# Kernel optimization log

Measured on AMD Instinct MI355X. Metric: run time of the kernel, lower is better.

Reference implementation:

```python
import jax, jax.numpy as jnp
import numpy as np

B, C, L = 16, 256, 4096
P, Q = 100, 20


def setup_inputs() -> dict:
    key = jax.random.key(0)
    k1, k2, k3, k4 = jax.random.split(key, 4)
    X = jax.random.normal(k1, (B, C, L), dtype=jnp.float32)
    projections = jax.random.normal(k2, (P, C), dtype=jnp.float32)
    # min < max per projection. Projected values ~ N(0, sqrt(C)), so scale ~ sqrt(C).
    scale = jnp.sqrt(jnp.float32(C))
    min_vals = -scale * (1.0 + jax.random.uniform(k3, (P,), dtype=jnp.float32))
    max_vals = scale * (1.0 + jax.random.uniform(k4, (P,), dtype=jnp.float32))
    return {"X": X, "projections": projections, "min_vals": min_vals, "max_vals": max_vals}


def reference(X, projections, min_vals, max_vals):
    # conv1d with kernel size 1 == per-position projection: [B,C,L] x [P,C] -> [B,P,L]
    a = jnp.einsum('bcl,pc->bpl', X, projections)
    # all quantile thresholds at once: thr[p,q] = min + (max-min)*(q+1)/(Q+1)
    fracs = (jnp.arange(1, Q + 1, dtype=jnp.float32)) / jnp.float32(Q + 1)  # [Q]
    thr = min_vals[:, None] + (max_vals - min_vals)[:, None] * fracs[None, :]  # [P,Q]
    # set[b,p,l,q] = a[b,p,l] < thr[p,q]
    set_ = (a[:, :, :, None] < thr[None, :, None, :]).astype(jnp.float32)  # [B,P,L,Q]
    cdf = jnp.mean(set_, axis=2)  # [B,P,Q]
    # transpose(2,1) -> [B,L,P,Q]; reshape -> [B,L,P*Q]; transpose(2,1) -> [B,P*Q,L]
    set_out = jnp.transpose(set_, (0, 2, 1, 3)).reshape(B, L, P * Q)
    set_out = jnp.transpose(set_out, (0, 2, 1))  # [B, P*Q, L]
    cdf_out = cdf.reshape(B, P * Q)
    return (cdf_out, set_out)
```

## Files before the change

kernel.cpp:

```cpp
#include <hip/hip_runtime.h>

#define Bsz 16
#define Cc  256
#define Ll  4096
#define Pp  100
#define Qq  20
#define PQ  (Pp * Qq)

#define LTILE 1024
#define NLT   (Ll / LTILE)
#define GP    10
#define NPG   (Pp / GP)
#define NXCD  8

typedef float f32x4 __attribute__((ext_vector_type(4)));

__global__ __launch_bounds__(256) void csf_main(
    const float* __restrict__ X,
    const float* __restrict__ proj,
    const float* __restrict__ mn,
    const float* __restrict__ mx,
    float* __restrict__ cdf,
    float* __restrict__ set_out) {
    const int id = blockIdx.x;
    const int x  = id & (NXCD - 1);
    const int k  = id >> 3;
    const int pg = k % NPG;
    const int gq = k / NPG;
    const int g  = gq * NXCD + x;
    const int lt = g & (NLT - 1);
    const int b  = g >> 2;

    const int tid = threadIdx.x;
    const int l0  = lt * LTILE + tid * 4;
    const int p0  = __builtin_amdgcn_readfirstlane(pg * GP);

    const float* Xb = X + (size_t)b * Cc * Ll + l0;

    float acc[GP][4];
#pragma unroll
    for (int i = 0; i < GP; i++)
#pragma unroll
        for (int kk = 0; kk < 4; kk++) acc[i][kk] = 0.0f;

#pragma unroll 4
    for (int c = 0; c < Cc; c++) {
        const f32x4 xv = *(const f32x4*)(Xb + (size_t)c * Ll);
#pragma unroll
        for (int i = 0; i < GP; i++) {
            const float w = proj[(size_t)(p0 + i) * Cc + c];
            acc[i][0] = __builtin_fmaf(xv.x, w, acc[i][0]);
            acc[i][1] = __builtin_fmaf(xv.y, w, acc[i][1]);
            acc[i][2] = __builtin_fmaf(xv.z, w, acc[i][2]);
            acc[i][3] = __builtin_fmaf(xv.w, w, acc[i][3]);
        }
    }

    float fr[Qq];
#pragma unroll
    for (int q = 0; q < Qq; q++) fr[q] = __fdiv_rn((float)(q + 1), 21.0f);

    float* ob = set_out + (size_t)b * PQ * Ll + l0;
    const bool lane0 = ((tid & 63) == 0);

#pragma unroll 1
    for (int i = 0; i < GP; i++) {
        const int p = p0 + i;
        const float mnp = mn[p];
        const float mxp = mx[p];
        const float d = __fsub_rn(mxp, mnp);
#pragma unroll
        for (int q = 0; q < Qq; q++) {
            const float thr = __fadd_rn(mnp, __fmul_rn(d, fr[q]));
            const bool b0 = acc[i][0] < thr;
            const bool b1 = acc[i][1] < thr;
            const bool b2 = acc[i][2] < thr;
            const bool b3 = acc[i][3] < thr;
            f32x4 o;
            o.x = b0 ? 1.0f : 0.0f;
            o.y = b1 ? 1.0f : 0.0f;
            o.z = b2 ? 1.0f : 0.0f;
            o.w = b3 ? 1.0f : 0.0f;
            __builtin_nontemporal_store(o, (f32x4*)(ob + (size_t)(p * Qq + q) * Ll));
            const int cnt = __popcll(__ballot(b0)) + __popcll(__ballot(b1))
                          + __popcll(__ballot(b2)) + __popcll(__ballot(b3));
            if (lane0) {
                atomicAdd(&cdf[(size_t)b * PQ + p * Qq + q],
                          (float)cnt * (1.0f / (float)Ll));
            }
        }
    }
}

extern "C" void kernel_launch(void* const* d_in, const int* in_sizes, int n_in,
                              void* d_out, int out_size, void* d_ws, size_t ws_size,
                              hipStream_t stream) {
    const float* X    = (const float*)d_in[0];
    const float* proj = (const float*)d_in[1];
    const float* mn   = (const float*)d_in[2];
    const float* mx   = (const float*)d_in[3];

    float* cdf     = (float*)d_out;
    float* set_out = cdf + (size_t)Bsz * PQ;

    (void)hipMemsetAsync(cdf, 0, (size_t)Bsz * PQ * sizeof(float), stream);

    csf_main<<<dim3(NLT * NPG * Bsz), 256, 0, stream>>>(X, proj, mn, mx, cdf,
                                                        set_out);
}
```

Baseline: 602.1 us.

## Split projection and thresholding into two kernels, stash projections in output buffer

Splits the fused kernel in two. The first kernel computes the projection and writes each value into the q=0 row of set_out, which serves as scratch space. The second kernel has one block per (b,p); it reads the full L row, writes all Q threshold rows, and reduces counts in shared memory into cdf with plain stores. This removes the memset and the per-wave atomics and gives full-row CDF reduction, but adds a write and re-read of the projections and a second launch. Reading row q=0 before overwriting it is safe only because each thread reads its own elements first.

```diff
diff --git a/kernel.cpp b/kernel.cpp
--- a/kernel.cpp
+++ b/kernel.cpp
@@ -15,96 +15,130 @@
 
 typedef float f32x4 __attribute__((ext_vector_type(4)));
 
-__global__ __launch_bounds__(256) void csf_main(
+
+__global__ __launch_bounds__(256) void csf_proj(
     const float* __restrict__ X,
     const float* __restrict__ proj,
+    float* __restrict__ set_out) {
+  const int id = blockIdx.x;
+  const int x  = id & (NXCD - 1);
+  const int k  = id >> 3;
+  const int pg = k % NPG;
+  const int gq = k / NPG;
+  const int g  = gq * NXCD + x;
+  const int lt = g & (NLT - 1);
+  const int b  = g >> 2;
+
+  const int tid = threadIdx.x;
+  const int l0  = lt * LTILE + tid * 4;
+  const int p0  = __builtin_amdgcn_readfirstlane(pg * GP);
+
+  const float* Xb = X + (size_t)b * Cc * Ll + l0;
+
+  float acc[GP][4];
+#pragma unroll
+  for (int i = 0; i < GP; i++)
+#pragma unroll
+    for (int kk = 0; kk < 4; kk++) acc[i][kk] = 0.0f;
+
+#pragma unroll 4
+  for (int c = 0; c < Cc; c++) {
+    const f32x4 xv = *(const f32x4*)(Xb + (size_t)c * Ll);
+#pragma unroll
+    for (int i = 0; i < GP; i++) {
+      const float w = proj[(size_t)(p0 + i) * Cc + c];
+      acc[i][0] = __builtin_fmaf(xv.x, w, acc[i][0]);
+      acc[i][1] = __builtin_fmaf(xv.y, w, acc[i][1]);
+      acc[i][2] = __builtin_fmaf(xv.z, w, acc[i][2]);
+      acc[i][3] = __builtin_fmaf(xv.w, w, acc[i][3]);
+    }
+  }
+
+  float* ob = set_out + (size_t)b * PQ * Ll + l0;
+#pragma unroll
+  for (int i = 0; i < GP; i++) {
+    f32x4 o;
+    o.x = acc[i][0]; o.y = acc[i][1]; o.z = acc[i][2]; o.w = acc[i][3];
+    *(f32x4*)(ob + (size_t)(p0 + i) * Qq * Ll) = o;
+  }
+}
+
+__global__ __launch_bounds__(256) void csf_thresh(
     const float* __restrict__ mn,
     const float* __restrict__ mx,
     float* __restrict__ cdf,
     float* __restrict__ set_out) {
-    const int id = blockIdx.x;
-    const int x  = id & (NXCD - 1);
-    const int k  = id >> 3;
-    const int pg = k % NPG;
-    const int gq = k / NPG;
-    const int g  = gq * NXCD + x;
-    const int lt = g & (NLT - 1);
-    const int b  = g >> 2;
+  const int id = blockIdx.x;
+  const int x  = id & (NXCD - 1);
+  const int k  = id >> 3;
+  const int hi = (k >= Pp) ? 1 : 0;
+  const int b  = 2 * x + hi;
+  const int p  = k - hi * Pp;
 
-    const int tid = threadIdx.x;
-    const int l0  = lt * LTILE + tid * 4;
-    const int p0  = __builtin_amdgcn_readfirstlane(pg * GP);
+  const int tid  = threadIdx.x;
+  const int wave = tid >> 6;
+  const int lane = tid & 63;
 
-    const float* Xb = X + (size_t)b * Cc * Ll + l0;
+  const float mnp = mn[p];
+  const float d   = __fsub_rn(mx[p], mnp);
 
-    float acc[GP][4];
+  const float FR[Qq] = {
+     1.0f/21.0f,  2.0f/21.0f,  3.0f/21.0f,  4.0f/21.0f,  5.0f/21.0f,
+     6.0f/21.0f,  7.0f/21.0f,  8.0f/21.0f,  9.0f/21.0f, 10.0f/21.0f,
+    11.0f/21.0f, 12.0f/21.0f, 13.0f/21.0f, 14.0f/21.0f, 15.0f/21.0f,
+    16.0f/21.0f, 17.0f/21.0f, 18.0f/21.0f, 19.0f/21.0f, 20.0f/21.0f };
+
+  float* rowbase = set_out + (size_t)b * PQ * Ll + (size_t)p * Qq * Ll;
+
+  int cnt[Qq];
 #pragma unroll
-    for (int i = 0; i < GP; i++)
-#pragma unroll
-        for (int kk = 0; kk < 4; kk++) acc[i][kk] = 0.0f;
-
-#pragma unroll 4
-    for (int c = 0; c < Cc; c++) {
-        const f32x4 xv = *(const f32x4*)(Xb + (size_t)c * Ll);
-#pragma unroll
-        for (int i = 0; i < GP; i++) {
-            const float w = proj[(size_t)(p0 + i) * Cc + c];
-            acc[i][0] = __builtin_fmaf(xv.x, w, acc[i][0]);
-            acc[i][1] = __builtin_fmaf(xv.y, w, acc[i][1]);
-            acc[i][2] = __builtin_fmaf(xv.z, w, acc[i][2]);
-            acc[i][3] = __builtin_fmaf(xv.w, w, acc[i][3]);
-        }
-    }
-
-    float fr[Qq];
-#pragma unroll
-    for (int q = 0; q < Qq; q++) fr[q] = __fdiv_rn((float)(q + 1), 21.0f);
-
-    float* ob = set_out + (size_t)b * PQ * Ll + l0;
-    const bool lane0 = ((tid & 63) == 0);
+  for (int q = 0; q < Qq; q++) cnt[q] = 0;
 
 #pragma unroll 1
-    for (int i = 0; i < GP; i++) {
-        const int p = p0 + i;
-        const float mnp = mn[p];
-        const float mxp = mx[p];
-        const float d = __fsub_rn(mxp, mnp);
+  for (int pass = 0; pass < 4; pass++) {
+    const int off = pass * 1024 + tid * 4;
+    const f32x4 a = *(const f32x4*)(rowbase + off);
 #pragma unroll
-        for (int q = 0; q < Qq; q++) {
-            const float thr = __fadd_rn(mnp, __fmul_rn(d, fr[q]));
-            const bool b0 = acc[i][0] < thr;
-            const bool b1 = acc[i][1] < thr;
-            const bool b2 = acc[i][2] < thr;
-            const bool b3 = acc[i][3] < thr;
-            f32x4 o;
-            o.x = b0 ? 1.0f : 0.0f;
-            o.y = b1 ? 1.0f : 0.0f;
-            o.z = b2 ? 1.0f : 0.0f;
-            o.w = b3 ? 1.0f : 0.0f;
-            __builtin_nontemporal_store(o, (f32x4*)(ob + (size_t)(p * Qq + q) * Ll));
-            const int cnt = __popcll(__ballot(b0)) + __popcll(__ballot(b1))
-                          + __popcll(__ballot(b2)) + __popcll(__ballot(b3));
-            if (lane0) {
-                atomicAdd(&cdf[(size_t)b * PQ + p * Qq + q],
-                          (float)cnt * (1.0f / (float)Ll));
-            }
-        }
+    for (int q = 0; q < Qq; q++) {
+      const float thr = __fadd_rn(mnp, __fmul_rn(d, FR[q]));
+      const bool b0 = a.x < thr;
+      const bool b1 = a.y < thr;
+      const bool b2 = a.z < thr;
+      const bool b3 = a.w < thr;
+      f32x4 o;
+      o.x = b0 ? 1.0f : 0.0f;
+      o.y = b1 ? 1.0f : 0.0f;
+      o.z = b2 ? 1.0f : 0.0f;
+      o.w = b3 ? 1.0f : 0.0f;
+      __builtin_nontemporal_store(o, (f32x4*)(rowbase + (size_t)q * Ll + off));
+      cnt[q] += __popcll(__ballot(b0)) + __popcll(__ballot(b1))
+              + __popcll(__ballot(b2)) + __popcll(__ballot(b3));
     }
+  }
+
+  __shared__ int sc[4][Qq];
+  if (lane == 0) {
+#pragma unroll
+    for (int q = 0; q < Qq; q++) sc[wave][q] = cnt[q];
+  }
+  __syncthreads();
+  if (tid < Qq) {
+    const int t = sc[0][tid] + sc[1][tid] + sc[2][tid] + sc[3][tid];
+    cdf[(size_t)b * PQ + p * Qq + tid] = (float)t * (1.0f / (float)Ll);
+  }
 }
 
 extern "C" void kernel_launch(void* const* d_in, const int* in_sizes, int n_in,
                               void* d_out, int out_size, void* d_ws, size_t ws_size,
                               hipStream_t stream) {
-    const float* X    = (const float*)d_in[0];
-    const float* proj = (const float*)d_in[1];
-    const float* mn   = (const float*)d_in[2];
-    const float* mx   = (const float*)d_in[3];
+  const float* X    = (const float*)d_in[0];
+  const float* proj = (const float*)d_in[1];
+  const float* mn   = (const float*)d_in[2];
+  const float* mx   = (const float*)d_in[3];
 
-    float* cdf     = (float*)d_out;
-    float* set_out = cdf + (size_t)Bsz * PQ;
+  float* cdf     = (float*)d_out;
+  float* set_out = cdf + (size_t)Bsz * PQ;
 
-    (void)hipMemsetAsync(cdf, 0, (size_t)Bsz * PQ * sizeof(float), stream);
-
-    csf_main<<<dim3(NLT * NPG * Bsz), 256, 0, stream>>>(X, proj, mn, mx, cdf,
-                                                        set_out);
+  csf_proj<<<dim3(NLT * NPG * Bsz), 256, 0, stream>>>(X, proj, set_out);
+  csf_thresh<<<dim3(Pp * Bsz), 256, 0, stream>>>(mn, mx, cdf, set_out);
 }
```

Result: no change. 598.5 us (-0.6%).
